# Performance work log

Measured on AMD Instinct MI355X. Metric: run time of the kernel, lower is better.

Reference implementation:

```python
import jax, jax.numpy as jnp
import numpy as np

H = 64      # LSTM hidden units
OUT = 10    # dense softmax classes


def setup_inputs() -> dict:
    key = jax.random.key(0)
    k0, k1, k2, k3 = jax.random.split(key, 4)
    B, T, D = 256, 1024, 128
    x = jax.random.normal(k0, (B, T, D), dtype=jnp.float32)
    # small weight scale keeps relu cell state stable over 1024 steps
    W = jax.random.normal(k1, (D, 4 * H), dtype=jnp.float32) * 0.05
    U = jax.random.normal(k2, (H, 4 * H), dtype=jnp.float32) * 0.05
    b = jnp.zeros((4 * H,), jnp.float32)
    Wd = jax.random.normal(k3, (H, OUT), dtype=jnp.float32) * 0.05
    bd = jnp.zeros((OUT,), jnp.float32)
    return {"x": x, "W": W, "U": U, "b": b, "Wd": Wd, "bd": bd}


def hard_sigmoid(z):
    # legacy Keras recurrent_activation default
    return jnp.clip(0.2 * z + 0.5, 0.0, 1.0)


def lstm_last_hidden(x, W, U, b):
    # x: [B,T,D] -> last hidden state [B,H]
    B = x.shape[0]
    xw = jnp.einsum('btd,dg->btg', x, W) + b  # [B,T,4H] input projection, computed once

    def step(carry, xt):
        h, c = carry
        z = xt + h @ U  # [B,4H]
        i = hard_sigmoid(z[:, :H])
        f = hard_sigmoid(z[:, H:2 * H])
        g = jax.nn.relu(z[:, 2 * H:3 * H])   # activation='relu' (candidate)
        o = hard_sigmoid(z[:, 3 * H:])
        c = f * c + i * g
        h = o * jax.nn.relu(c)               # activation='relu' on cell output
        return (h, c), None

    h0 = jnp.zeros((B, H), x.dtype)
    (h, _), _ = jax.lax.scan(step, (h0, h0), jnp.swapaxes(xw, 0, 1))
    return h


def reference(x, W, U, b, Wd, bd):
    h = lstm_last_hidden(x, W, U, b)          # [B,H]
    return jax.nn.softmax(h @ Wd + bd, axis=-1)  # [B,OUT]
```

## Files before the change

kernel.cpp:

```cpp
#include <hip/hip_runtime.h>
#include <hip/hip_bf16.h>

#define Hh   64
#define G4   256
#define Dd   128
#define Bsz  256
#define Tt   1024
#define NOUT 10

typedef __bf16  bf16x8 __attribute__((ext_vector_type(8)));
typedef __bf16  bf16x4 __attribute__((ext_vector_type(4)));
typedef float   f32x4v __attribute__((ext_vector_type(4)));

__device__ __forceinline__ int rho_origcol(int rho) {
    const int g  = rho >> 6;
    const int s  = (rho >> 5) & 1;
    const int d2 = (rho >> 4) & 1;
    const int kq = (rho >> 2) & 3;
    const int dl = rho & 3;
    return g * 64 + (32 * s + 8 * kq + 4 * d2 + dl);
}


__device__ __forceinline__ void gld_lds16(const void* g, void* l) {
    __builtin_amdgcn_global_load_lds(
        (const __attribute__((address_space(1))) unsigned int*)g,
        (__attribute__((address_space(3))) unsigned int*)l, 16, 0, 0);
}

__global__ __launch_bounds__(128)
void k0_prep(const float* __restrict__ W, const float* __restrict__ b,
             __bf16* __restrict__ Wt, float* __restrict__ bias2) {
    const int rho = blockIdx.x;
    const int k   = threadIdx.x;
    const int col = rho_origcol(rho);
    const bool isg = ((rho >> 6) == 2);
    const float sc = isg ? 1.f : 0.2f;
    Wt[(size_t)rho * Dd + k] = (__bf16)(sc * W[(size_t)k * G4 + col]);
    if (k == 0) bias2[rho] = sc * b[col] + (isg ? 0.f : 0.5f);
}

#define K1_RT 8

__global__ __launch_bounds__(256)
void k1_mfma(const float* __restrict__ x, const __bf16* __restrict__ Wt,
             const float* __restrict__ bias, __bf16* __restrict__ xws) {
    const int tid = threadIdx.x;
    const int w   = tid >> 6;
    const int l   = tid & 63;
    const int r16 = l & 15;
    const int kq  = l >> 4;
    const size_t rowbase = (size_t)blockIdx.x * (16 * K1_RT);

    const int bb = (int)(rowbase >> 10);
    const size_t gm_base = ((size_t)(bb >> 4) << 23);
    const int lane_off = w * 512 + (r16 >> 2) * 128 + (bb & 15) * 8 + (r16 & 3) * 2;

    bf16x8 bfr[4][4];
    float  bval[4];
#pragma unroll
    for (int ct = 0; ct < 4; ++ct) {
        const int col = w * 64 + ct * 16 + r16;
        const __bf16* wp = Wt + (size_t)col * Dd + kq * 8;
#pragma unroll
        for (int kk = 0; kk < 4; ++kk)
            bfr[ct][kk] = *(const bf16x8*)(wp + kk * 32);
        bval[ct] = bias[col];
    }

    for (int rt = 0; rt < K1_RT; ++rt) {
        const size_t arow = rowbase + rt * 16 + r16;
        const float* xr = x + arow * Dd + kq * 8;
        bf16x8 afr[4];
#pragma unroll
        for (int kk = 0; kk < 4; ++kk) {
            const float4 lo = *(const float4*)(xr + kk * 32);
            const float4 hi = *(const float4*)(xr + kk * 32 + 4);
            afr[kk][0] = (__bf16)lo.x; afr[kk][1] = (__bf16)lo.y;
            afr[kk][2] = (__bf16)lo.z; afr[kk][3] = (__bf16)lo.w;
            afr[kk][4] = (__bf16)hi.x; afr[kk][5] = (__bf16)hi.y;
            afr[kk][6] = (__bf16)hi.z; afr[kk][7] = (__bf16)hi.w;
        }
        f32x4v acc[4];
#pragma unroll
        for (int ct = 0; ct < 4; ++ct)
            acc[ct] = (f32x4v){bval[ct], bval[ct], bval[ct], bval[ct]};
#pragma unroll
        for (int ct = 0; ct < 4; ++ct)
#pragma unroll
            for (int kk = 0; kk < 4; ++kk)
                acc[ct] = __builtin_amdgcn_mfma_f32_16x16x32_bf16(
                              afr[kk], bfr[ct][kk], acc[ct], 0, 0, 0);

        const int trow0 = (int)((rowbase + rt * 16 + kq * 4) & 1023);
#pragma unroll
        for (int ct = 0; ct < 4; ++ct) {
#pragma unroll
            for (int rr = 0; rr < 4; ++rr) {
                char* dst = (char*)xws + gm_base + (size_t)(trow0 + rr) * 8192
                            + (size_t)ct * 2048 + lane_off;
                *(__bf16*)dst = (__bf16)acc[ct][rr];
            }
        }
    }
}

#define SST 8

__global__ __launch_bounds__(256, 1)
void k2_scan(const __bf16* __restrict__ xws, const float* __restrict__ U,
             float* __restrict__ hout) {
    const int tid = threadIdx.x;
    const int w   = tid >> 6;
    const int l   = tid & 63;
    const int kq  = l >> 4;
    const int m   = l & 15;
    const int s_  = w >> 1, d2 = w & 1;
    const int G   = blockIdx.x;

    __shared__ __align__(16) unsigned char ring[4][2][SST][2048];
    __shared__ __align__(16) __bf16 hx[2][16][72];

    bf16x8 au[4][2];
#pragma unroll
    for (int g = 0; g < 4; ++g) {
        const float sc = (g == 2) ? 1.f : 0.2f;
        const int col = rho_origcol(64 * g + 16 * w + m);
#pragma unroll
        for (int ks = 0; ks < 2; ++ks)
#pragma unroll
            for (int j = 0; j < 8; ++j)
                au[g][ks][j] = (__bf16)(sc * U[(size_t)(ks * 32 + kq * 8 + j) * G4 + col]);
    }

    float c4[4]  = {0.f, 0.f, 0.f, 0.f};
    float hv4[4] = {0.f, 0.f, 0.f, 0.f};

    {
        const bf16x4 z4 = {(__bf16)0.f, (__bf16)0.f, (__bf16)0.f, (__bf16)0.f};
        *(bf16x4*)&hx[1][m][32 * s_ + 8 * kq + 4 * d2] = z4;
    }

    const char* gl = (const char*)xws + ((size_t)G << 23)
                     + (size_t)w * 2048 + (size_t)l * 16;

#pragma unroll
    for (int buf = 0; buf < 2; ++buf)
#pragma unroll
        for (int stp = 0; stp < SST; ++stp)
#pragma unroll
            for (int gg = 0; gg < 2; ++gg)
                gld_lds16(gl + (size_t)(buf * SST + stp) * 8192 + gg * 1024,
                          &ring[w][buf][stp][gg * 1024]);
    __syncthreads();

    uint2  dz[4];
    f32x4v accN[4];
    bf16x8 bh0, bh1;

    for (int S = 0; S < Tt / SST; ++S) {
        const int cur = S & 1;

        asm volatile("s_waitcnt vmcnt(16)" ::: "memory");
        __builtin_amdgcn_sched_barrier(0);

#pragma unroll
        for (int g = 0; g < 4; ++g)
            dz[g] = *(const uint2*)&ring[w][cur][0][g * 512 + kq * 128 + m * 8];
#pragma unroll
        for (int g = 0; g < 4; ++g) {
            accN[g][0] = __builtin_bit_cast(float, dz[g].x << 16);
            accN[g][1] = __builtin_bit_cast(float, dz[g].x & 0xFFFF0000u);
            accN[g][2] = __builtin_bit_cast(float, dz[g].y << 16);
            accN[g][3] = __builtin_bit_cast(float, dz[g].y & 0xFFFF0000u);
        }

#pragma unroll
        for (int stp = 0; stp < SST; ++stp) {
            const int rp = (stp + 1) & 1;

            bh0 = *(const bf16x8*)&hx[rp][m][8 * kq];
            bh1 = *(const bf16x8*)&hx[rp][m][32 + 8 * kq];

            f32x4v acc[4];
#pragma unroll
            for (int g = 0; g < 4; ++g) {
                acc[g] = __builtin_amdgcn_mfma_f32_16x16x32_bf16(au[g][0], bh0, accN[g], 0, 0, 0);
                acc[g] = __builtin_amdgcn_mfma_f32_16x16x32_bf16(au[g][1], bh1, acc[g], 0, 0, 0);
            }

            bf16x4 hb;
#pragma unroll
            for (int r = 0; r < 4; ++r) {
                const float gi = __builtin_amdgcn_fmed3f(acc[0][r], 0.f, 1.f);
                const float gf = __builtin_amdgcn_fmed3f(acc[1][r], 0.f, 1.f);
                const float gg = fmaxf(acc[2][r], 0.f);
                const float go = __builtin_amdgcn_fmed3f(acc[3][r], 0.f, 1.f);
                c4[r] = fmaf(gf, c4[r], gi * gg);
                hv4[r] = go * fmaxf(c4[r], 0.f);
                hb[r] = (__bf16)hv4[r];
            }

            *(bf16x4*)&hx[stp & 1][m][32 * s_ + 8 * kq + 4 * d2] = hb;

            if (stp < SST - 1) {
#pragma unroll
                for (int g = 0; g < 4; ++g)
                    dz[g] = *(const uint2*)&ring[w][cur][stp + 1][g * 512
                                                                  + kq * 128 + m * 8];
                asm volatile("s_waitcnt lgkmcnt(4)" ::: "memory");
            } else {
                asm volatile("s_waitcnt lgkmcnt(0)" ::: "memory");
            }
            __builtin_amdgcn_sched_barrier(0);
            __builtin_amdgcn_s_barrier();
            __builtin_amdgcn_sched_barrier(0);

            if (stp < SST - 1) {
#pragma unroll
                for (int g = 0; g < 4; ++g) {
                    accN[g][0] = __builtin_bit_cast(float, dz[g].x << 16);
                    accN[g][1] = __builtin_bit_cast(float, dz[g].x & 0xFFFF0000u);
                    accN[g][2] = __builtin_bit_cast(float, dz[g].y << 16);
                    accN[g][3] = __builtin_bit_cast(float, dz[g].y & 0xFFFF0000u);
                }
            }
        }

        {
            int tn0 = (S + 2) * SST;
            if (tn0 > Tt - SST) tn0 = Tt - SST;
            const char* p = gl + (size_t)tn0 * 8192;
#pragma unroll
            for (int stp = 0; stp < SST; ++stp)
#pragma unroll
                for (int gg = 0; gg < 2; ++gg)
                    gld_lds16(p + (size_t)stp * 8192 + gg * 1024,
                              &ring[w][cur][stp][gg * 1024]);
        }
    }

#pragma unroll
    for (int r = 0; r < 4; ++r)
        hout[(size_t)(G * 16 + m) * Hh + 32 * s_ + 8 * kq + 4 * d2 + r] = hv4[r];
}

__global__ __launch_bounds__(256)
void k3_dense(const float* __restrict__ hin, const float* __restrict__ Wd,
              const float* __restrict__ bd, float* __restrict__ out) {
    __shared__ float wd[Hh * NOUT];
    __shared__ float bds[NOUT];
    for (int i = threadIdx.x; i < Hh * NOUT; i += blockDim.x) wd[i] = Wd[i];
    if (threadIdx.x < NOUT) bds[threadIdx.x] = bd[threadIdx.x];
    __syncthreads();

    const int r = threadIdx.x;
    if (r < Bsz) {
        float hrow[Hh];
#pragma unroll
        for (int j = 0; j < Hh; ++j) hrow[j] = hin[(size_t)r * Hh + j];
        float logits[NOUT];
#pragma unroll
        for (int o = 0; o < NOUT; ++o) {
            float acc = bds[o];
#pragma unroll
            for (int j = 0; j < Hh; ++j) acc = fmaf(hrow[j], wd[j * NOUT + o], acc);
            logits[o] = acc;
        }
        float mx = logits[0];
#pragma unroll
        for (int o = 1; o < NOUT; ++o) mx = fmaxf(mx, logits[o]);
        float s = 0.f;
#pragma unroll
        for (int o = 0; o < NOUT; ++o) { logits[o] = expf(logits[o] - mx); s += logits[o]; }
        const float inv = 1.f / s;
#pragma unroll
        for (int o = 0; o < NOUT; ++o) out[(size_t)r * NOUT + o] = logits[o] * inv;
    }
}

extern "C" void kernel_launch(void* const* d_in, const int* in_sizes, int n_in,
                              void* d_out, int out_size, void* d_ws, size_t ws_size,
                              hipStream_t stream) {
    const float* x  = (const float*)d_in[0];
    const float* W  = (const float*)d_in[1];
    const float* U  = (const float*)d_in[2];
    const float* b  = (const float*)d_in[3];
    const float* Wd = (const float*)d_in[4];
    const float* bd = (const float*)d_in[5];
    float* out = (float*)d_out;

    const size_t xw_bytes = (size_t)Bsz * Tt * G4 * sizeof(__bf16);
    __bf16* xws   = (__bf16*)d_ws;
    float*  hbuf  = (float*)((char*)d_ws + xw_bytes);
    __bf16* Wt    = (__bf16*)((char*)hbuf + (size_t)Bsz * Hh * sizeof(float));
    float*  bias2 = (float*)((char*)Wt + (size_t)G4 * Dd * sizeof(__bf16));

    k0_prep<<<G4, Dd, 0, stream>>>(W, b, Wt, bias2);
    k1_mfma<<<(Bsz * Tt) / (16 * K1_RT), 256, 0, stream>>>(x, Wt, bias2, xws);
    k2_scan<<<Bsz / 16, 256, 0, stream>>>(xws, U, hbuf);
    k3_dense<<<1, 256, 0, stream>>>(hbuf, Wd, bd, out);
}
```

Before: 560.9 us.

## Store input projection row-major and swizzle LDS ring in scan kernel

```diff
diff --git a/kernel.cpp b/kernel.cpp
--- a/kernel.cpp
+++ b/kernel.cpp
@@ -44,17 +44,13 @@
 
 __global__ __launch_bounds__(256)
 void k1_mfma(const float* __restrict__ x, const __bf16* __restrict__ Wt,
-             const float* __restrict__ bias, __bf16* __restrict__ xws) {
+             const float* __restrict__ bias, __bf16* __restrict__ xw) {
     const int tid = threadIdx.x;
     const int w   = tid >> 6;
     const int l   = tid & 63;
     const int r16 = l & 15;
     const int kq  = l >> 4;
     const size_t rowbase = (size_t)blockIdx.x * (16 * K1_RT);
-
-    const int bb = (int)(rowbase >> 10);
-    const size_t gm_base = ((size_t)(bb >> 4) << 23);
-    const int lane_off = w * 512 + (r16 >> 2) * 128 + (bb & 15) * 8 + (r16 & 3) * 2;
 
     bf16x8 bfr[4][4];
     float  bval[4];
@@ -92,15 +88,13 @@
                 acc[ct] = __builtin_amdgcn_mfma_f32_16x16x32_bf16(
                               afr[kk], bfr[ct][kk], acc[ct], 0, 0, 0);
 
-        const int trow0 = (int)((rowbase + rt * 16 + kq * 4) & 1023);
+        const size_t orow0 = rowbase + rt * 16 + kq * 4;
 #pragma unroll
         for (int ct = 0; ct < 4; ++ct) {
-#pragma unroll
-            for (int rr = 0; rr < 4; ++rr) {
-                char* dst = (char*)xws + gm_base + (size_t)(trow0 + rr) * 8192
-                            + (size_t)ct * 2048 + lane_off;
-                *(__bf16*)dst = (__bf16)acc[ct][rr];
-            }
+            const int col = w * 64 + ct * 16 + r16;
+#pragma unroll
+            for (int rr = 0; rr < 4; ++rr)
+                xw[(orow0 + rr) * G4 + col] = (__bf16)acc[ct][rr];
         }
     }
 }
@@ -108,7 +102,7 @@
 #define SST 8
 
 __global__ __launch_bounds__(256, 1)
-void k2_scan(const __bf16* __restrict__ xws, const float* __restrict__ U,
+void k2_scan(const __bf16* __restrict__ xw, const float* __restrict__ U,
              float* __restrict__ hout) {
     const int tid = threadIdx.x;
     const int w   = tid >> 6;
@@ -118,7 +112,7 @@
     const int s_  = w >> 1, d2 = w & 1;
     const int G   = blockIdx.x;
 
-    __shared__ __align__(16) unsigned char ring[4][2][SST][2048];
+    __shared__ __align__(16) unsigned char ring[2][SST][8192];
     __shared__ __align__(16) __bf16 hx[2][16][72];
 
     bf16x8 au[4][2];
@@ -141,17 +135,29 @@
         *(bf16x4*)&hx[1][m][32 * s_ + 8 * kq + 4 * d2] = z4;
     }
 
-    const char* gl = (const char*)xws + ((size_t)G << 23)
-                     + (size_t)w * 2048 + (size_t)l * 16;
+    const char* xwc = (const char*)xw;
+    const char* src_j[2];
+#pragma unroll
+    for (int j = 0; j < 2; ++j) {
+        const int i  = 2 * w + j;
+        const int mp = 2 * i + (l >> 5);
+        const int sch = ((l & 31) - mp) & 31;
+        src_j[j] = xwc + (size_t)(16 * G + mp) * 524288 + (size_t)sch * 16;
+    }
+    int rd_off[4];
+#pragma unroll
+    for (int g = 0; g < 4; ++g)
+        rd_off[g] = m * 512 + (((8 * g + 2 * w + (kq >> 1) + m) & 31) << 4)
+                    + ((kq & 1) << 3);
 
 #pragma unroll
     for (int buf = 0; buf < 2; ++buf)
 #pragma unroll
         for (int stp = 0; stp < SST; ++stp)
 #pragma unroll
-            for (int gg = 0; gg < 2; ++gg)
-                gld_lds16(gl + (size_t)(buf * SST + stp) * 8192 + gg * 1024,
-                          &ring[w][buf][stp][gg * 1024]);
+            for (int j = 0; j < 2; ++j)
+                gld_lds16(src_j[j] + (size_t)(buf * SST + stp) * 512,
+                          &ring[buf][stp][(2 * w + j) * 1024]);
     __syncthreads();
 
     uint2  dz[4];
@@ -163,10 +169,12 @@
 
         asm volatile("s_waitcnt vmcnt(16)" ::: "memory");
         __builtin_amdgcn_sched_barrier(0);
+        __builtin_amdgcn_s_barrier();
+        __builtin_amdgcn_sched_barrier(0);
 
 #pragma unroll
         for (int g = 0; g < 4; ++g)
-            dz[g] = *(const uint2*)&ring[w][cur][0][g * 512 + kq * 128 + m * 8];
+            dz[g] = *(const uint2*)&ring[cur][0][rd_off[g]];
 #pragma unroll
         for (int g = 0; g < 4; ++g) {
             accN[g][0] = __builtin_bit_cast(float, dz[g].x << 16);
@@ -206,8 +214,7 @@
             if (stp < SST - 1) {
 #pragma unroll
                 for (int g = 0; g < 4; ++g)
-                    dz[g] = *(const uint2*)&ring[w][cur][stp + 1][g * 512
-                                                                  + kq * 128 + m * 8];
+                    dz[g] = *(const uint2*)&ring[cur][stp + 1][rd_off[g]];
                 asm volatile("s_waitcnt lgkmcnt(4)" ::: "memory");
             } else {
                 asm volatile("s_waitcnt lgkmcnt(0)" ::: "memory");
@@ -230,13 +237,12 @@
         {
             int tn0 = (S + 2) * SST;
             if (tn0 > Tt - SST) tn0 = Tt - SST;
-            const char* p = gl + (size_t)tn0 * 8192;
 #pragma unroll
             for (int stp = 0; stp < SST; ++stp)
 #pragma unroll
-                for (int gg = 0; gg < 2; ++gg)
-                    gld_lds16(p + (size_t)stp * 8192 + gg * 1024,
-                              &ring[w][cur][stp][gg * 1024]);
+                for (int j = 0; j < 2; ++j)
+                    gld_lds16(src_j[j] + (size_t)(tn0 + stp) * 512,
+                              &ring[cur][stp][(2 * w + j) * 1024]);
         }
     }
 
@@ -291,13 +297,13 @@
     float* out = (float*)d_out;
 
     const size_t xw_bytes = (size_t)Bsz * Tt * G4 * sizeof(__bf16);
-    __bf16* xws   = (__bf16*)d_ws;
+    __bf16* xw    = (__bf16*)d_ws;
     float*  hbuf  = (float*)((char*)d_ws + xw_bytes);
     __bf16* Wt    = (__bf16*)((char*)hbuf + (size_t)Bsz * Hh * sizeof(float));
     float*  bias2 = (float*)((char*)Wt + (size_t)G4 * Dd * sizeof(__bf16));
 
     k0_prep<<<G4, Dd, 0, stream>>>(W, b, Wt, bias2);
-    k1_mfma<<<(Bsz * Tt) / (16 * K1_RT), 256, 0, stream>>>(x, Wt, bias2, xws);
-    k2_scan<<<Bsz / 16, 256, 0, stream>>>(xws, U, hbuf);
+    k1_mfma<<<(Bsz * Tt) / (16 * K1_RT), 256, 0, stream>>>(x, Wt, bias2, xw);
+    k2_scan<<<Bsz / 16, 256, 0, stream>>>(xw, U, hbuf);
     k3_dense<<<1, 256, 0, stream>>>(hbuf, Wd, bd, out);
 }
```

After: 547.8 us, median of 2. 1.02x faster.
